# Kernel optimization log

Hardware: AMD Instinct MI355X
Metric: run time of the kernel (lower is better)

Reference implementation:

```python
import jax, jax.numpy as jnp
import numpy as np

D_MODEL = 1024
N_HEAD = 16


def setup_inputs() -> dict:
    key = jax.random.key(0)
    ks = jax.random.split(key, 11)
    B, S, D = 2, 2048, D_MODEL
    scale = 1.0 / np.sqrt(D)
    inp = {
        "query_tensor": jax.random.normal(ks[0], (B, S, D), jnp.float32),
        "key_tensor": jax.random.normal(ks[1], (B, S, D), jnp.float32),
        "value_tensor": jax.random.normal(ks[2], (B, S, D), jnp.float32),
        "w_q": jax.random.normal(ks[3], (D, D), jnp.float32) * scale,
        "b_q": jnp.zeros((D,), jnp.float32),
        "w_k": jax.random.normal(ks[4], (D, D), jnp.float32) * scale,
        "b_k": jnp.zeros((D,), jnp.float32),
        "w_v": jax.random.normal(ks[5], (D, D), jnp.float32) * scale,
        "b_v": jnp.zeros((D,), jnp.float32),
        "w_out": jax.random.normal(ks[6], (D, D), jnp.float32) * scale,
        "b_out": jnp.zeros((D,), jnp.float32),
    }
    return inp


def _split_heads(x, n_head):
    b, s, d = x.shape
    return x.reshape(b, s, n_head, d // n_head).transpose(0, 2, 1, 3)  # [b,h,s,dk]


def reference(query_tensor, key_tensor, value_tensor, w_q, b_q, w_k, b_k, w_v, b_v, w_out, b_out):
    # torch Linear: y = x @ W.T + b
    q = query_tensor @ w_q.T + b_q
    k = key_tensor @ w_k.T + b_k
    v = value_tensor @ w_v.T + b_v
    q = _split_heads(q, N_HEAD)
    k = _split_heads(k, N_HEAD)
    v = _split_heads(v, N_HEAD)
    d_k = k.shape[-1]
    scores = jnp.einsum("bhqd,bhkd->bhqk", q, k) / jnp.sqrt(jnp.float32(d_k))
    attn = jax.nn.softmax(scores, axis=-1)
    ctx = jnp.einsum("bhqk,bhkd->bhqd", attn, v)
    b, h, s, dk = ctx.shape
    ctx = ctx.transpose(0, 2, 1, 3).reshape(b, s, h * dk)
    return ctx @ w_out.T + b_out
```

## Files before the change

kernel.cpp:

```cpp
#include <hip/hip_runtime.h>
#include <hip/hip_bf16.h>

using ushort = unsigned short;

typedef __attribute__((ext_vector_type(8))) short bf16x8;
typedef __attribute__((ext_vector_type(4))) float f32x4;
typedef __attribute__((ext_vector_type(16))) float f32x16;
typedef __attribute__((ext_vector_type(4))) unsigned short u16x4;

#define DEVINL __device__ __forceinline__


static constexpr size_t WQ_O = 12582912;
static constexpr size_t WO_O = 15728640;
static constexpr size_t QB_O = 16777216;
static constexpr size_t KB_O = 20971520;
static constexpr size_t VT_O = 25165824;
static constexpr size_t CTX_O = 0;

DEVINL ushort f2bf(float f) {
  unsigned u = __builtin_bit_cast(unsigned, f);
  u += 0x7fffu + ((u >> 16) & 1u);
  return (ushort)(u >> 16);
}

DEVINL void gld16(const ushort* g, ushort* lds) {
  __builtin_amdgcn_global_load_lds(
      (const __attribute__((address_space(1))) void*)g,
      (__attribute__((address_space(3))) void*)lds, 16, 0, 0);
}

DEVINL void barrier_war() {
  __builtin_amdgcn_sched_barrier(0);
  asm volatile("" ::: "memory");
  __builtin_amdgcn_s_barrier();
  __builtin_amdgcn_sched_barrier(0);
}
DEVINL void barrier_raw() {
  __builtin_amdgcn_sched_barrier(0);
  asm volatile("s_waitcnt lgkmcnt(0)" ::: "memory");
  __builtin_amdgcn_sched_barrier(0);
  __builtin_amdgcn_s_barrier();
  __builtin_amdgcn_sched_barrier(0);
}

__global__ __launch_bounds__(256) void cvt_w(
    const float* __restrict__ wq, const float* __restrict__ wk,
    const float* __restrict__ wv, const float* __restrict__ wo,
    ushort* __restrict__ ws)
{
  int e = (blockIdx.x * 256 + threadIdx.x) * 8;
  const float* s;
  if      (e < 1048576) s = wq + e;
  else if (e < 2097152) s = wk + (e - 1048576);
  else if (e < 3145728) s = wv + (e - 2097152);
  else                  s = wo + (e - 3145728);
  float4 a = *(const float4*)s;
  float4 b = *(const float4*)(s + 4);
  union { u16x4 v; ushort u[4]; } r0, r1;
  r0.u[0] = f2bf(a.x); r0.u[1] = f2bf(a.y); r0.u[2] = f2bf(a.z); r0.u[3] = f2bf(a.w);
  r1.u[0] = f2bf(b.x); r1.u[1] = f2bf(b.y); r1.u[2] = f2bf(b.z); r1.u[3] = f2bf(b.w);
  *(u16x4*)(ws + WQ_O + e) = r0.v;
  *(u16x4*)(ws + WQ_O + e + 4) = r1.v;
}

template<bool CVTA, int BN>
DEVINL void gemm_core(const void* __restrict__ Av, const ushort* __restrict__ Bw,
                      const float* __restrict__ bias, void* __restrict__ Cout,
                      float scale, int omode, int row0, int col0)
{
  constexpr int K = 1024;
  constexpr int BI = BN / 32;
  constexpr int NJ = BN / 32;
  __shared__ ushort As[128 * 64];
  __shared__ ushort Bs[BN * 64];
  const int t = threadIdx.x;
  const int l = t & 63;
  const int w = t >> 6;
  const int wr = w >> 1, wc = w & 1;

  const int srow = t >> 3;
  const int scol8 = (t & 7) * 8;
  const int swz_half = ((((t & 7) * 16) ^ ((srow & 7) << 4)) >> 1);

  const ushort* Ap16 = (const ushort*)Av + (size_t)(row0 + srow) * K + scol8;
  const float*  Ap32 = (const float*)Av + (size_t)(row0 + srow) * K + scol8;
  const ushort* Bp = Bw + (size_t)(col0 + srow) * K + scol8;

  bf16x8 areg[4], breg[BI];
  float4 a32[4][2];
  auto loadstage = [&](int k0) {
#pragma unroll
    for (int i = 0; i < 4; ++i) {
      if constexpr (CVTA) {
        a32[i][0] = *(const float4*)(Ap32 + (size_t)(i * 32) * K + k0);
        a32[i][1] = *(const float4*)(Ap32 + (size_t)(i * 32) * K + k0 + 4);
      } else {
        areg[i] = *(const bf16x8*)(Ap16 + (size_t)(i * 32) * K + k0);
      }
    }
#pragma unroll
    for (int i = 0; i < BI; ++i)
      breg[i] = *(const bf16x8*)(Bp + (size_t)(i * 32) * K + k0);
  };

  f32x4 acc[4][NJ];
#pragma unroll
  for (int i = 0; i < 4; ++i)
#pragma unroll
    for (int j = 0; j < NJ; ++j) acc[i][j] = (f32x4){0.f, 0.f, 0.f, 0.f};

  loadstage(0);
#pragma unroll 1
  for (int kt = 0; kt < K / 64; ++kt) {
    barrier_war();
#pragma unroll
    for (int i = 0; i < 4; ++i) {
      if constexpr (CVTA) {
        union { bf16x8 v; unsigned u[4]; } pk;
        asm("v_cvt_pk_bf16_f32 %0, %1, %2" : "=v"(pk.u[0]) : "v"(a32[i][0].x), "v"(a32[i][0].y));
        asm("v_cvt_pk_bf16_f32 %0, %1, %2" : "=v"(pk.u[1]) : "v"(a32[i][0].z), "v"(a32[i][0].w));
        asm("v_cvt_pk_bf16_f32 %0, %1, %2" : "=v"(pk.u[2]) : "v"(a32[i][1].x), "v"(a32[i][1].y));
        asm("v_cvt_pk_bf16_f32 %0, %1, %2" : "=v"(pk.u[3]) : "v"(a32[i][1].z), "v"(a32[i][1].w));
        *(bf16x8*)&As[(srow + i * 32) * 64 + swz_half] = pk.v;
      } else {
        *(bf16x8*)&As[(srow + i * 32) * 64 + swz_half] = areg[i];
      }
    }
#pragma unroll
    for (int i = 0; i < BI; ++i)
      *(bf16x8*)&Bs[(srow + i * 32) * 64 + swz_half] = breg[i];
    if (kt + 1 < K / 64) loadstage((kt + 1) * 64);
    barrier_raw();
#pragma unroll
    for (int ks = 0; ks < 2; ++ks) {
      bf16x8 af[4], bfr[NJ];
#pragma unroll
      for (int mi = 0; mi < 4; ++mi) {
        int r = wr * 64 + mi * 16 + (l & 15);
        int cb = ((ks << 6) | ((l >> 4) << 4)) ^ ((r & 7) << 4);
        af[mi] = *(const bf16x8*)&As[r * 64 + (cb >> 1)];
      }
#pragma unroll
      for (int nj = 0; nj < NJ; ++nj) {
        int r = wc * (BN / 2) + nj * 16 + (l & 15);
        int cb = ((ks << 6) | ((l >> 4) << 4)) ^ ((r & 7) << 4);
        bfr[nj] = *(const bf16x8*)&Bs[r * 64 + (cb >> 1)];
      }
#pragma unroll
      for (int mi = 0; mi < 4; ++mi)
#pragma unroll
        for (int nj = 0; nj < NJ; ++nj)
          acc[mi][nj] = __builtin_amdgcn_mfma_f32_16x16x32_bf16(af[mi], bfr[nj], acc[mi][nj], 0, 0, 0);
    }
  }

  const int cl = l & 15;
#pragma unroll
  for (int mi = 0; mi < 4; ++mi) {
#pragma unroll
    for (int nj = 0; nj < NJ; ++nj) {
      int n = col0 + wc * (BN / 2) + nj * 16 + cl;
      float bv = bias[n];
      int mbase = row0 + wr * 64 + mi * 16 + (l >> 4) * 4;
      if (omode == 1) {
        float* Of = (float*)Cout;
#pragma unroll
        for (int ri = 0; ri < 4; ++ri)
          Of[(size_t)(mbase + ri) * 1024 + n] = (acc[mi][nj][ri] + bv) * scale;
      } else if (omode == 0) {
        ushort* Ob = (ushort*)Cout;
        int h = n >> 6, d = n & 63;
#pragma unroll
        for (int ri = 0; ri < 4; ++ri) {
          int m = mbase + ri;
          int b = m >> 11, s = m & 2047;
          Ob[(size_t)((b * 16 + h) * 2048 + s) * 64 + d] = f2bf((acc[mi][nj][ri] + bv) * scale);
        }
      } else {
        ushort* Ob = (ushort*)Cout;
        int h = n >> 6, d = n & 63;
        int b = mbase >> 11, s = mbase & 2047;
        union { u16x4 v; ushort u[4]; } pk;
#pragma unroll
        for (int ri = 0; ri < 4; ++ri) pk.u[ri] = f2bf((acc[mi][nj][ri] + bv) * scale);
        *(u16x4*)&Ob[(size_t)((b * 16 + h) * 64 + d) * 2048 + s] = pk.v;
      }
    }
  }
}

__global__ __launch_bounds__(256, 2) void gemm_qkv(
    const float* __restrict__ xq, const float* __restrict__ xk, const float* __restrict__ xv,
    const ushort* __restrict__ ws_c, ushort* __restrict__ ws_m,
    const float* __restrict__ bq, const float* __restrict__ bk, const float* __restrict__ bv)
{
  const int hw = blockIdx.x + 8 * blockIdx.y + 256 * blockIdx.z;
  const int X = hw & 7, j = hw >> 3;
  const int g = 8 * (j >> 3) + X;
  const int bx = j & 7;
  const int by = g & 31, z = g >> 5;

  const float* A = (z == 0) ? xq : ((z == 1) ? xk : xv);
  const ushort* W = ws_c + WQ_O + (size_t)z * 1048576;
  const float* bias = (z == 0) ? bq : ((z == 1) ? bk : bv);
  ushort* dst = ws_m + QB_O + (size_t)z * 4194304;
  float scale = (z == 0) ? (0.125f * 1.4426950408889634f) : 1.0f;
  int omode = (z == 2) ? 2 : 0;
  gemm_core<true, 128>(A, W, bias, dst, scale, omode, by * 128, bx * 128);
}

__global__ __launch_bounds__(256, 2) void gemm_out(
    const ushort* __restrict__ ctx, const ushort* __restrict__ wo,
    const float* __restrict__ bo, float* __restrict__ out)
{
  gemm_core<false, 64>(ctx, wo, bo, out, 1.0f, 1, blockIdx.y * 128, blockIdx.x * 64);
}

__global__ __launch_bounds__(512, 4) void attn8(
    const ushort* __restrict__ Qb, const ushort* __restrict__ Kb,
    const ushort* __restrict__ Vtb, ushort* __restrict__ Ctx)
{
  __shared__ ushort smem[32768];

  const int t = threadIdx.x, l = t & 63, w = t >> 6;
  const int wq4 = w & 3, half = w >> 2;
  const int hi2 = l >> 5, q = l & 31;

  const int hw = blockIdx.y * 16 + blockIdx.x;
  const int j = hw >> 3;
  const int bh = (hw & 7) + 8 * (j >> 4);
  const int qt = j & 15;

  const int kvb = half * 1024;
  const ushort* Qp = Qb + ((size_t)bh * 2048 + qt * 128 + wq4 * 32) * 64;
  const ushort* Kp = Kb + (size_t)bh * 2048 * 64;
  const ushort* Vp = Vtb + (size_t)bh * 64 * 2048;

  ushort* Ksh = smem + half * 8192;
  ushort* Vsh = smem + 16384 + half * 8192;

  bf16x8 qf[4];
#pragma unroll
  for (int ks = 0; ks < 4; ++ks)
    qf[ks] = *(const bf16x8*)(Qp + q * 64 + ks * 16 + hi2 * 8);

  auto stageKV = [&](int pp, int kv0) {
#pragma unroll
    for (int i = 0; i < 2; ++i) {
      int R = (i * 4 + wq4) * 8 + (l >> 3);
      int g = l & 7;
      int sR = (R & ~12) | ((R & 4) << 1) | ((R & 8) >> 1);
      gld16(Kp + (size_t)(kv0 + sR) * 64 + (g ^ (R & 7)) * 8,
            Ksh + pp * 4096 + (i * 4 + wq4) * 512);
      gld16(Vp + (size_t)R * 2048 + kv0 + (g ^ (R & 7)) * 8,
            Vsh + pp * 4096 + (i * 4 + wq4) * 512);
    }
  };

  f32x16 acc0, acc1;
#pragma unroll
  for (int i = 0; i < 16; ++i) { acc0[i] = 0.f; acc1[i] = 0.f; }
  f32x16 Zv;
#pragma unroll
  for (int i = 0; i < 16; ++i) Zv[i] = 0.f;
  float lrun = 0.f;

  const int rsw = (q & 7) << 4;

  stageKV(0, kvb);
  __syncthreads();

#pragma unroll 1
  for (int kt = 0; kt < 16; ++kt) {
    const int p = kt & 1;
    const ushort* Kl = Ksh + p * 4096;
    const ushort* Vl = Vsh + p * 4096;

    f32x16 scA, scB;
    __builtin_amdgcn_s_setprio(1);
    {
      bf16x8 kf = *(const bf16x8*)&Kl[q * 64 + (((hi2 * 16)) ^ rsw) / 2];
      scA = __builtin_amdgcn_mfma_f32_32x32x16_bf16(kf, qf[0], Zv, 0, 0, 0);
#pragma unroll
      for (int ks = 1; ks < 4; ++ks) {
        bf16x8 k2 = *(const bf16x8*)&Kl[q * 64 + (((ks * 32 + hi2 * 16) ^ rsw) >> 1)];
        scA = __builtin_amdgcn_mfma_f32_32x32x16_bf16(k2, qf[ks], scA, 0, 0, 0);
      }
      const int r1 = (32 + q) * 64;
      bf16x8 kg = *(const bf16x8*)&Kl[r1 + (((hi2 * 16)) ^ rsw) / 2];
      scB = __builtin_amdgcn_mfma_f32_32x32x16_bf16(kg, qf[0], Zv, 0, 0, 0);
#pragma unroll
      for (int ks = 1; ks < 4; ++ks) {
        bf16x8 k2 = *(const bf16x8*)&Kl[r1 + (((ks * 32 + hi2 * 16) ^ rsw) >> 1)];
        scB = __builtin_amdgcn_mfma_f32_32x32x16_bf16(k2, qf[ks], scB, 0, 0, 0);
      }
    }
    __builtin_amdgcn_s_setprio(0);

    if (kt + 1 < 16) stageKV(p ^ 1, kvb + (kt + 1) * 64);

#pragma unroll
    for (int c = 0; c < 2; ++c) {
      f32x16& sc = (c == 0) ? scA : scB;
      float s0 = 0.f, s1 = 0.f, s2 = 0.f, s3 = 0.f;
#pragma unroll
      for (int i = 0; i < 4; ++i) {
        float e0 = __builtin_amdgcn_exp2f(sc[i]);      sc[i] = e0;      s0 += e0;
        float e1 = __builtin_amdgcn_exp2f(sc[4 + i]);  sc[4 + i] = e1;  s1 += e1;
        float e2 = __builtin_amdgcn_exp2f(sc[8 + i]);  sc[8 + i] = e2;  s2 += e2;
        float e3 = __builtin_amdgcn_exp2f(sc[12 + i]); sc[12 + i] = e3; s3 += e3;
      }
      lrun += (s0 + s1) + (s2 + s3);

      union PU { bf16x8 v; unsigned u[4]; } pA, pB;
#pragma unroll
      for (int i = 0; i < 4; ++i) {
        asm("v_cvt_pk_bf16_f32 %0, %1, %2" : "=v"(pA.u[i]) : "v"(sc[2 * i]), "v"(sc[2 * i + 1]));
        asm("v_cvt_pk_bf16_f32 %0, %1, %2" : "=v"(pB.u[i]) : "v"(sc[8 + 2 * i]), "v"(sc[9 + 2 * i]));
      }

      __builtin_amdgcn_s_setprio(1);
#pragma unroll
      for (int db = 0; db < 2; ++db) {
        const int d = db * 32 + q;
        bf16x8 va = *(const bf16x8*)&Vl[d * 64 + (((c * 64 + hi2 * 16) ^ rsw) >> 1)];
        bf16x8 vb = *(const bf16x8*)&Vl[d * 64 + (((c * 64 + 32 + hi2 * 16) ^ rsw) >> 1)];
        if (db == 0) {
          acc0 = __builtin_amdgcn_mfma_f32_32x32x16_bf16(va, pA.v, acc0, 0, 0, 0);
          acc0 = __builtin_amdgcn_mfma_f32_32x32x16_bf16(vb, pB.v, acc0, 0, 0, 0);
        } else {
          acc1 = __builtin_amdgcn_mfma_f32_32x32x16_bf16(va, pA.v, acc1, 0, 0, 0);
          acc1 = __builtin_amdgcn_mfma_f32_32x32x16_bf16(vb, pB.v, acc1, 0, 0, 0);
        }
      }
      __builtin_amdgcn_s_setprio(0);
    }
    __syncthreads();
  }

  float lsum = lrun + __shfl_xor(lrun, 32);
  float* Lf = (float*)smem;

  if (l < 32) Lf[half * 128 + wq4 * 32 + q] = lsum;
  __syncthreads();
  const float inv = 1.0f / (Lf[wq4 * 32 + q] + Lf[128 + wq4 * 32 + q]);
  __syncthreads();

  auto mrg = [&](int row, int G) -> float* {
    return Lf + row * 64 + ((G ^ (row & 15)) << 2);
  };

  if (half == 1) {
    const int row = wq4 * 32 + q;
#pragma unroll
    for (int db = 0; db < 2; ++db)
#pragma unroll
      for (int g = 0; g < 4; ++g) {
        float4 v;
        if (db == 0) v = (float4){acc0[g * 4], acc0[g * 4 + 1], acc0[g * 4 + 2], acc0[g * 4 + 3]};
        else         v = (float4){acc1[g * 4], acc1[g * 4 + 1], acc1[g * 4 + 2], acc1[g * 4 + 3]};
        *(float4*)mrg(row, db * 8 + g * 2 + hi2) = v;
      }
  }
  __syncthreads();

  if (half == 0) {
    const int row = wq4 * 32 + q;
#pragma unroll
    for (int db = 0; db < 2; ++db)
#pragma unroll
      for (int g = 0; g < 4; ++g) {
        float* p = mrg(row, db * 8 + g * 2 + hi2);
        float4 pv = *(float4*)p;
        float4 o;
        if (db == 0) o = (float4){(acc0[g * 4] + pv.x) * inv, (acc0[g * 4 + 1] + pv.y) * inv,
                                  (acc0[g * 4 + 2] + pv.z) * inv, (acc0[g * 4 + 3] + pv.w) * inv};
        else         o = (float4){(acc1[g * 4] + pv.x) * inv, (acc1[g * 4 + 1] + pv.y) * inv,
                                  (acc1[g * 4 + 2] + pv.z) * inv, (acc1[g * 4 + 3] + pv.w) * inv};
        *(float4*)p = o;
      }
  }
  __syncthreads();

  {
    const int b = bh >> 4, h = bh & 15;
    const int d0 = (l & 7) * 8;
#pragma unroll
    for (int rr = 0; rr < 2; ++rr) {
      int row = w * 16 + rr * 8 + (l >> 3);
      float4 f0 = *(const float4*)mrg(row, (l & 7) * 2);
      float4 f1 = *(const float4*)mrg(row, (l & 7) * 2 + 1);
      union { u16x4 v; ushort u[4]; } o0, o1;
      o0.u[0] = f2bf(f0.x); o0.u[1] = f2bf(f0.y); o0.u[2] = f2bf(f0.z); o0.u[3] = f2bf(f0.w);
      o1.u[0] = f2bf(f1.x); o1.u[1] = f2bf(f1.y); o1.u[2] = f2bf(f1.z); o1.u[3] = f2bf(f1.w);
      ushort* dst = Ctx + ((size_t)b * 2048 + qt * 128 + row) * 1024 + h * 64 + d0;
      *(u16x4*)dst = o0.v;
      *(u16x4*)(dst + 4) = o1.v;
    }
  }
}

extern "C" void kernel_launch(void* const* d_in, const int* in_sizes, int n_in,
                              void* d_out, int out_size, void* d_ws, size_t ws_size,
                              hipStream_t stream) {
  const float* xq = (const float*)d_in[0];
  const float* xk = (const float*)d_in[1];
  const float* xv = (const float*)d_in[2];
  const float* wq = (const float*)d_in[3];
  const float* bq = (const float*)d_in[4];
  const float* wk = (const float*)d_in[5];
  const float* bk = (const float*)d_in[6];
  const float* wv = (const float*)d_in[7];
  const float* bv = (const float*)d_in[8];
  const float* wo = (const float*)d_in[9];
  const float* bo = (const float*)d_in[10];
  ushort* ws = (ushort*)d_ws;

  cvt_w<<<2048, 256, 0, stream>>>(wq, wk, wv, wo, ws);
  gemm_qkv<<<dim3(8, 32, 3), 256, 0, stream>>>(xq, xk, xv, ws, ws, bq, bk, bv);
  attn8<<<dim3(16, 32), 512, 0, stream>>>(ws + QB_O, ws + KB_O, ws + VT_O, ws + CTX_O);
  gemm_out<<<dim3(16, 32), 256, 0, stream>>>(ws + CTX_O, ws + WO_O, bo, (float*)d_out);
}
```

Measured before the change: 104.7 us.

## Double-buffer GEMM tiles with direct global-to-LDS loads and partial vmcnt waits

```diff
diff --git a/kernel.cpp b/kernel.cpp
--- a/kernel.cpp
+++ b/kernel.cpp
@@ -36,9 +36,37 @@
   __builtin_amdgcn_s_barrier();
   __builtin_amdgcn_sched_barrier(0);
 }
-DEVINL void barrier_raw() {
-  __builtin_amdgcn_sched_barrier(0);
-  asm volatile("s_waitcnt lgkmcnt(0)" ::: "memory");
+DEVINL void barrier_lgkm_vm20() {
+  __builtin_amdgcn_sched_barrier(0);
+  asm volatile("s_waitcnt vmcnt(20) lgkmcnt(0)" ::: "memory");
+  __builtin_amdgcn_sched_barrier(0);
+  __builtin_amdgcn_s_barrier();
+  __builtin_amdgcn_sched_barrier(0);
+}
+DEVINL void barrier_lgkm_vm12() {
+  __builtin_amdgcn_sched_barrier(0);
+  asm volatile("s_waitcnt vmcnt(12) lgkmcnt(0)" ::: "memory");
+  __builtin_amdgcn_sched_barrier(0);
+  __builtin_amdgcn_s_barrier();
+  __builtin_amdgcn_sched_barrier(0);
+}
+DEVINL void barrier_lgkm_vm0() {
+  __builtin_amdgcn_sched_barrier(0);
+  asm volatile("s_waitcnt vmcnt(0) lgkmcnt(0)" ::: "memory");
+  __builtin_amdgcn_sched_barrier(0);
+  __builtin_amdgcn_s_barrier();
+  __builtin_amdgcn_sched_barrier(0);
+}
+DEVINL void barrier_vm6() {
+  __builtin_amdgcn_sched_barrier(0);
+  asm volatile("s_waitcnt vmcnt(6)" ::: "memory");
+  __builtin_amdgcn_sched_barrier(0);
+  __builtin_amdgcn_s_barrier();
+  __builtin_amdgcn_sched_barrier(0);
+}
+DEVINL void barrier_vm0() {
+  __builtin_amdgcn_sched_barrier(0);
+  asm volatile("s_waitcnt vmcnt(0)" ::: "memory");
   __builtin_amdgcn_sched_barrier(0);
   __builtin_amdgcn_s_barrier();
   __builtin_amdgcn_sched_barrier(0);
@@ -64,137 +92,14 @@
   *(u16x4*)(ws + WQ_O + e + 4) = r1.v;
 }
 
-template<bool CVTA, int BN>
-DEVINL void gemm_core(const void* __restrict__ Av, const ushort* __restrict__ Bw,
-                      const float* __restrict__ bias, void* __restrict__ Cout,
-                      float scale, int omode, int row0, int col0)
-{
-  constexpr int K = 1024;
-  constexpr int BI = BN / 32;
-  constexpr int NJ = BN / 32;
-  __shared__ ushort As[128 * 64];
-  __shared__ ushort Bs[BN * 64];
-  const int t = threadIdx.x;
-  const int l = t & 63;
-  const int w = t >> 6;
-  const int wr = w >> 1, wc = w & 1;
-
-  const int srow = t >> 3;
-  const int scol8 = (t & 7) * 8;
-  const int swz_half = ((((t & 7) * 16) ^ ((srow & 7) << 4)) >> 1);
-
-  const ushort* Ap16 = (const ushort*)Av + (size_t)(row0 + srow) * K + scol8;
-  const float*  Ap32 = (const float*)Av + (size_t)(row0 + srow) * K + scol8;
-  const ushort* Bp = Bw + (size_t)(col0 + srow) * K + scol8;
-
-  bf16x8 areg[4], breg[BI];
-  float4 a32[4][2];
-  auto loadstage = [&](int k0) {
-#pragma unroll
-    for (int i = 0; i < 4; ++i) {
-      if constexpr (CVTA) {
-        a32[i][0] = *(const float4*)(Ap32 + (size_t)(i * 32) * K + k0);
-        a32[i][1] = *(const float4*)(Ap32 + (size_t)(i * 32) * K + k0 + 4);
-      } else {
-        areg[i] = *(const bf16x8*)(Ap16 + (size_t)(i * 32) * K + k0);
-      }
-    }
-#pragma unroll
-    for (int i = 0; i < BI; ++i)
-      breg[i] = *(const bf16x8*)(Bp + (size_t)(i * 32) * K + k0);
-  };
-
-  f32x4 acc[4][NJ];
-#pragma unroll
-  for (int i = 0; i < 4; ++i)
-#pragma unroll
-    for (int j = 0; j < NJ; ++j) acc[i][j] = (f32x4){0.f, 0.f, 0.f, 0.f};
-
-  loadstage(0);
-#pragma unroll 1
-  for (int kt = 0; kt < K / 64; ++kt) {
-    barrier_war();
-#pragma unroll
-    for (int i = 0; i < 4; ++i) {
-      if constexpr (CVTA) {
-        union { bf16x8 v; unsigned u[4]; } pk;
-        asm("v_cvt_pk_bf16_f32 %0, %1, %2" : "=v"(pk.u[0]) : "v"(a32[i][0].x), "v"(a32[i][0].y));
-        asm("v_cvt_pk_bf16_f32 %0, %1, %2" : "=v"(pk.u[1]) : "v"(a32[i][0].z), "v"(a32[i][0].w));
-        asm("v_cvt_pk_bf16_f32 %0, %1, %2" : "=v"(pk.u[2]) : "v"(a32[i][1].x), "v"(a32[i][1].y));
-        asm("v_cvt_pk_bf16_f32 %0, %1, %2" : "=v"(pk.u[3]) : "v"(a32[i][1].z), "v"(a32[i][1].w));
-        *(bf16x8*)&As[(srow + i * 32) * 64 + swz_half] = pk.v;
-      } else {
-        *(bf16x8*)&As[(srow + i * 32) * 64 + swz_half] = areg[i];
-      }
-    }
-#pragma unroll
-    for (int i = 0; i < BI; ++i)
-      *(bf16x8*)&Bs[(srow + i * 32) * 64 + swz_half] = breg[i];
-    if (kt + 1 < K / 64) loadstage((kt + 1) * 64);
-    barrier_raw();
-#pragma unroll
-    for (int ks = 0; ks < 2; ++ks) {
-      bf16x8 af[4], bfr[NJ];
-#pragma unroll
-      for (int mi = 0; mi < 4; ++mi) {
-        int r = wr * 64 + mi * 16 + (l & 15);
-        int cb = ((ks << 6) | ((l >> 4) << 4)) ^ ((r & 7) << 4);
-        af[mi] = *(const bf16x8*)&As[r * 64 + (cb >> 1)];
-      }
-#pragma unroll
-      for (int nj = 0; nj < NJ; ++nj) {
-        int r = wc * (BN / 2) + nj * 16 + (l & 15);
-        int cb = ((ks << 6) | ((l >> 4) << 4)) ^ ((r & 7) << 4);
-        bfr[nj] = *(const bf16x8*)&Bs[r * 64 + (cb >> 1)];
-      }
-#pragma unroll
-      for (int mi = 0; mi < 4; ++mi)
-#pragma unroll
-        for (int nj = 0; nj < NJ; ++nj)
-          acc[mi][nj] = __builtin_amdgcn_mfma_f32_16x16x32_bf16(af[mi], bfr[nj], acc[mi][nj], 0, 0, 0);
-    }
-  }
-
-  const int cl = l & 15;
-#pragma unroll
-  for (int mi = 0; mi < 4; ++mi) {
-#pragma unroll
-    for (int nj = 0; nj < NJ; ++nj) {
-      int n = col0 + wc * (BN / 2) + nj * 16 + cl;
-      float bv = bias[n];
-      int mbase = row0 + wr * 64 + mi * 16 + (l >> 4) * 4;
-      if (omode == 1) {
-        float* Of = (float*)Cout;
-#pragma unroll
-        for (int ri = 0; ri < 4; ++ri)
-          Of[(size_t)(mbase + ri) * 1024 + n] = (acc[mi][nj][ri] + bv) * scale;
-      } else if (omode == 0) {
-        ushort* Ob = (ushort*)Cout;
-        int h = n >> 6, d = n & 63;
-#pragma unroll
-        for (int ri = 0; ri < 4; ++ri) {
-          int m = mbase + ri;
-          int b = m >> 11, s = m & 2047;
-          Ob[(size_t)((b * 16 + h) * 2048 + s) * 64 + d] = f2bf((acc[mi][nj][ri] + bv) * scale);
-        }
-      } else {
-        ushort* Ob = (ushort*)Cout;
-        int h = n >> 6, d = n & 63;
-        int b = mbase >> 11, s = mbase & 2047;
-        union { u16x4 v; ushort u[4]; } pk;
-#pragma unroll
-        for (int ri = 0; ri < 4; ++ri) pk.u[ri] = f2bf((acc[mi][nj][ri] + bv) * scale);
-        *(u16x4*)&Ob[(size_t)((b * 16 + h) * 64 + d) * 2048 + s] = pk.v;
-      }
-    }
-  }
-}
-
 __global__ __launch_bounds__(256, 2) void gemm_qkv(
     const float* __restrict__ xq, const float* __restrict__ xk, const float* __restrict__ xv,
     const ushort* __restrict__ ws_c, ushort* __restrict__ ws_m,
     const float* __restrict__ bq, const float* __restrict__ bk, const float* __restrict__ bv)
 {
+  __shared__ ushort As[128 * 64];
+  __shared__ ushort Bs[2][128 * 64];
+
   const int hw = blockIdx.x + 8 * blockIdx.y + 256 * blockIdx.z;
   const int X = hw & 7, j = hw >> 3;
   const int g = 8 * (j >> 3) + X;
@@ -205,16 +110,219 @@
   const ushort* W = ws_c + WQ_O + (size_t)z * 1048576;
   const float* bias = (z == 0) ? bq : ((z == 1) ? bk : bv);
   ushort* dst = ws_m + QB_O + (size_t)z * 4194304;
-  float scale = (z == 0) ? (0.125f * 1.4426950408889634f) : 1.0f;
-  int omode = (z == 2) ? 2 : 0;
-  gemm_core<true, 128>(A, W, bias, dst, scale, omode, by * 128, bx * 128);
+  const float scale = (z == 0) ? (0.125f * 1.4426950408889634f) : 1.0f;
+  const int omode = (z == 2) ? 2 : 0;
+  const int row0 = by * 128, col0 = bx * 128;
+
+  const int t = threadIdx.x, l = t & 63, w = t >> 6;
+  const int wr = w >> 1, wc = w & 1;
+  const int srow = t >> 3;
+  const int scol8 = (t & 7) * 8;
+  const int swz_half = ((((t & 7) * 16) ^ ((srow & 7) << 4)) >> 1);
+
+  const float* Ap32 = A + (size_t)(row0 + srow) * 1024 + scol8;
+
+  auto gldB = [&](int pp, int k0) {
+#pragma unroll
+    for (int i = 0; i < 4; ++i) {
+      int R = (i * 4 + w) * 8 + (l >> 3);
+      int gg = l & 7;
+      gld16(W + (size_t)(col0 + R) * 1024 + k0 + (gg ^ (R & 7)) * 8,
+            (ushort*)&Bs[pp][(i * 4 + w) * 512]);
+    }
+  };
+
+  float4 aA[4][2], aB[4][2];
+  auto loadA = [&](float4 (&d)[4][2], int k0) {
+#pragma unroll
+    for (int i = 0; i < 4; ++i) {
+      d[i][0] = *(const float4*)(Ap32 + (size_t)(i * 32) * 1024 + k0);
+      d[i][1] = *(const float4*)(Ap32 + (size_t)(i * 32) * 1024 + k0 + 4);
+    }
+  };
+  auto writeA = [&](const float4 (&s)[4][2]) {
+#pragma unroll
+    for (int i = 0; i < 4; ++i) {
+      union { bf16x8 v; unsigned u[4]; } pk;
+      asm("v_cvt_pk_bf16_f32 %0, %1, %2" : "=v"(pk.u[0]) : "v"(s[i][0].x), "v"(s[i][0].y));
+      asm("v_cvt_pk_bf16_f32 %0, %1, %2" : "=v"(pk.u[1]) : "v"(s[i][0].z), "v"(s[i][0].w));
+      asm("v_cvt_pk_bf16_f32 %0, %1, %2" : "=v"(pk.u[2]) : "v"(s[i][1].x), "v"(s[i][1].y));
+      asm("v_cvt_pk_bf16_f32 %0, %1, %2" : "=v"(pk.u[3]) : "v"(s[i][1].z), "v"(s[i][1].w));
+      *(bf16x8*)&As[(srow + i * 32) * 64 + swz_half] = pk.v;
+    }
+  };
+
+  f32x4 acc[4][4];
+#pragma unroll
+  for (int i = 0; i < 4; ++i)
+#pragma unroll
+    for (int jj = 0; jj < 4; ++jj) acc[i][jj] = (f32x4){0.f, 0.f, 0.f, 0.f};
+
+  auto mfma_phase = [&](const ushort* Bl) {
+#pragma unroll
+    for (int ks = 0; ks < 2; ++ks) {
+      bf16x8 af[4], bfr[4];
+#pragma unroll
+      for (int mi = 0; mi < 4; ++mi) {
+        int r = wr * 64 + mi * 16 + (l & 15);
+        int cb = ((ks << 6) | ((l >> 4) << 4)) ^ ((r & 7) << 4);
+        af[mi] = *(const bf16x8*)&As[r * 64 + (cb >> 1)];
+      }
+#pragma unroll
+      for (int nj = 0; nj < 4; ++nj) {
+        int r = wc * 64 + nj * 16 + (l & 15);
+        int cb = ((ks << 6) | ((l >> 4) << 4)) ^ ((r & 7) << 4);
+        bfr[nj] = *(const bf16x8*)&Bl[r * 64 + (cb >> 1)];
+      }
+#pragma unroll
+      for (int mi = 0; mi < 4; ++mi)
+#pragma unroll
+        for (int nj = 0; nj < 4; ++nj)
+          acc[mi][nj] = __builtin_amdgcn_mfma_f32_16x16x32_bf16(af[mi], bfr[nj], acc[mi][nj], 0, 0, 0);
+    }
+  };
+
+  gldB(0, 0);
+  loadA(aA, 0);
+  loadA(aB, 64);
+
+#pragma unroll 1
+  for (int kt2 = 0; kt2 < 14; kt2 += 2) {
+    barrier_war();
+    gldB(1, (kt2 + 1) * 64);
+    writeA(aA);
+    loadA(aA, (kt2 + 2) * 64);
+    barrier_lgkm_vm20();
+    mfma_phase(Bs[0]);
+    barrier_war();
+    gldB(0, (kt2 + 2) * 64);
+    writeA(aB);
+    loadA(aB, (kt2 + 3) * 64);
+    barrier_lgkm_vm20();
+    mfma_phase(Bs[1]);
+  }
+  barrier_war();
+  gldB(1, 15 * 64);
+  writeA(aA);
+  barrier_lgkm_vm12();
+  mfma_phase(Bs[0]);
+  barrier_war();
+  writeA(aB);
+  barrier_lgkm_vm0();
+  mfma_phase(Bs[1]);
+
+  const int cl = l & 15;
+#pragma unroll
+  for (int mi = 0; mi < 4; ++mi) {
+#pragma unroll
+    for (int nj = 0; nj < 4; ++nj) {
+      int n = col0 + wc * 64 + nj * 16 + cl;
+      float bv = bias[n];
+      int mbase = row0 + wr * 64 + mi * 16 + (l >> 4) * 4;
+      if (omode == 0) {
+        int h = n >> 6, d = n & 63;
+#pragma unroll
+        for (int ri = 0; ri < 4; ++ri) {
+          int m = mbase + ri;
+          int b = m >> 11, s = m & 2047;
+          dst[(size_t)((b * 16 + h) * 2048 + s) * 64 + d] = f2bf((acc[mi][nj][ri] + bv) * scale);
+        }
+      } else {
+        int h = n >> 6, d = n & 63;
+        int b = mbase >> 11, s = mbase & 2047;
+        union { u16x4 v; ushort u[4]; } pk;
+#pragma unroll
+        for (int ri = 0; ri < 4; ++ri) pk.u[ri] = f2bf((acc[mi][nj][ri] + bv) * scale);
+        *(u16x4*)&dst[(size_t)((b * 16 + h) * 64 + d) * 2048 + s] = pk.v;
+      }
+    }
+  }
 }
 
 __global__ __launch_bounds__(256, 2) void gemm_out(
     const ushort* __restrict__ ctx, const ushort* __restrict__ wo,
     const float* __restrict__ bo, float* __restrict__ out)
 {
-  gemm_core<false, 64>(ctx, wo, bo, out, 1.0f, 1, blockIdx.y * 128, blockIdx.x * 64);
+  __shared__ ushort As2[2][128 * 64];
+  __shared__ ushort Bs2[2][64 * 64];
+
+  const int row0 = blockIdx.y * 128, col0 = blockIdx.x * 64;
+  const int t = threadIdx.x, l = t & 63, w = t >> 6;
+  const int wr = w >> 1, wc = w & 1;
+
+  auto gldAB = [&](int pp, int k0) {
+#pragma unroll
+    for (int i = 0; i < 4; ++i) {
+      int R = (i * 4 + w) * 8 + (l >> 3);
+      int gg = l & 7;
+      gld16(ctx + (size_t)(row0 + R) * 1024 + k0 + (gg ^ (R & 7)) * 8,
+            (ushort*)&As2[pp][(i * 4 + w) * 512]);
+    }
+#pragma unroll
+    for (int i = 0; i < 2; ++i) {
+      int R = (i * 4 + w) * 8 + (l >> 3);
+      int gg = l & 7;
+      gld16(wo + (size_t)(col0 + R) * 1024 + k0 + (gg ^ (R & 7)) * 8,
+            (ushort*)&Bs2[pp][(i * 4 + w) * 512]);
+    }
+  };
+
+  f32x4 acc[4][2];
+#pragma unroll
+  for (int i = 0; i < 4; ++i)
+#pragma unroll
+    for (int jj = 0; jj < 2; ++jj) acc[i][jj] = (f32x4){0.f, 0.f, 0.f, 0.f};
+
+  auto mfma_phase = [&](const ushort* Al, const ushort* Bl) {
+#pragma unroll
+    for (int ks = 0; ks < 2; ++ks) {
+      bf16x8 af[4], bfr[2];
+#pragma unroll
+      for (int mi = 0; mi < 4; ++mi) {
+        int r = wr * 64 + mi * 16 + (l & 15);
+        int cb = ((ks << 6) | ((l >> 4) << 4)) ^ ((r & 7) << 4);
+        af[mi] = *(const bf16x8*)&Al[r * 64 + (cb >> 1)];
+      }
+#pragma unroll
+      for (int nj = 0; nj < 2; ++nj) {
+        int r = wc * 32 + nj * 16 + (l & 15);
+        int cb = ((ks << 6) | ((l >> 4) << 4)) ^ ((r & 7) << 4);
+        bfr[nj] = *(const bf16x8*)&Bl[r * 64 + (cb >> 1)];
+      }
+#pragma unroll
+      for (int mi = 0; mi < 4; ++mi)
+#pragma unroll
+        for (int nj = 0; nj < 2; ++nj)
+          acc[mi][nj] = __builtin_amdgcn_mfma_f32_16x16x32_bf16(af[mi], bfr[nj], acc[mi][nj], 0, 0, 0);
+    }
+  };
+
+  gldAB(0, 0);
+#pragma unroll 1
+  for (int kt = 0; kt < 15; ++kt) {
+    const int p = kt & 1;
+    barrier_war();
+    gldAB(p ^ 1, (kt + 1) * 64);
+    barrier_vm6();
+    mfma_phase(As2[p], Bs2[p]);
+  }
+  barrier_war();
+  barrier_vm0();
+  mfma_phase(As2[1], Bs2[1]);
+
+  const int cl = l & 15;
+#pragma unroll
+  for (int mi = 0; mi < 4; ++mi) {
+#pragma unroll
+    for (int nj = 0; nj < 2; ++nj) {
+      int n = col0 + wc * 32 + nj * 16 + cl;
+      float bv = bo[n];
+      int mbase = row0 + wr * 64 + mi * 16 + (l >> 4) * 4;
+#pragma unroll
+      for (int ri = 0; ri < 4; ++ri)
+        out[(size_t)(mbase + ri) * 1024 + n] = acc[mi][nj][ri] + bv;
+    }
+  }
 }
 
 __global__ __launch_bounds__(512, 4) void attn8(
```

After: 112.8 us. 7.7% more time.
